# Performance work log

Hardware: AMD Instinct MI355X
Metric: run time of the kernel (lower is better)

Reference implementation:

```python
import jax, jax.numpy as jnp
import numpy as np

B, N, IN_DIM, HID, EMB, E = 64, 2048, 128, 256, 64, 4194304
TOTAL = B * N


def _init(key, shape, fan_in):
    return jax.random.normal(key, shape, jnp.float32) / np.sqrt(fan_in).astype(np.float32)


def setup_inputs() -> dict:
    key = jax.random.key(0)
    ks = jax.random.split(key, 9)
    x = jax.random.normal(ks[0], (TOTAL, IN_DIM), jnp.float32)
    src = jax.random.randint(ks[1], (E,), 0, TOTAL)
    dst = jax.random.randint(ks[2], (E,), 0, TOTAL)
    return {
        "x": x,
        "src": src,
        "dst": dst,
        "num_nodes": TOTAL,
        "nodes_per_graph": N,
        "w_lin": _init(ks[3], (IN_DIM, HID), IN_DIM),
        "b_lin": jnp.zeros((HID,), jnp.float32),
        "w_c0": _init(ks[4], (HID, HID), HID),
        "b_c0": jnp.zeros((HID,), jnp.float32),
        "w_c1": _init(ks[5], (HID, HID), HID),
        "b_c1": jnp.zeros((HID,), jnp.float32),
        "w_emb": _init(ks[6], (HID, EMB), HID),
        "b_emb": jnp.zeros((EMB,), jnp.float32),
    }


def reference(x, src, dst, num_nodes, nodes_per_graph,
              w_lin, b_lin, w_c0, b_c0, w_c1, b_c1, w_emb, b_emb):
    # DGL GraphConv norm='both': deg clamped to min 1, symmetric normalization
    ones = jnp.ones(src.shape, x.dtype)
    out_deg = jax.ops.segment_sum(ones, src, num_segments=num_nodes)
    in_deg = jax.ops.segment_sum(ones, dst, num_segments=num_nodes)
    out_norm = jnp.maximum(out_deg, 1.0) ** -0.5  # [num_nodes]
    in_norm = jnp.maximum(in_deg, 1.0) ** -0.5

    def graph_conv(h, W, b):
        hs = h * out_norm[:, None]                                   # pre-norm by out-degree
        agg = jax.ops.segment_sum(hs[src], dst, num_segments=num_nodes)  # SpMM: sum messages
        return (agg * in_norm[:, None]) @ W + b                      # post-norm, then weight

    h = jax.nn.relu(x @ w_lin + b_lin)          # [total, HID]
    h = jax.nn.relu(graph_conv(h, w_c0, b_c0))  # residual=False for agg_style='node'
    h = jax.nn.relu(graph_conv(h, w_c1, b_c1))
    # agent node 0 of each graph in the batch: indices 0, N, 2N, ...
    agent = h[jnp.arange(0, num_nodes, nodes_per_graph)]  # [B, HID]
    return agent @ w_emb + b_emb                          # [B, EMB]
```

## Files before the change

kernel.cpp:

```cpp
#include <hip/hip_runtime.h>
#include <hip/hip_bf16.h>

#define TOTAL_N   131072
#define NEDGE     4194304
#define NPG       2048
#define IN_DIM_K  128
#define HID_K     256
#define EMB_K     64
#define NAGENT    64

#define F1CAP     4096
#define APACK     128
#define BCAP      96
#define NL        8

#define G1        256
#define EPB1      (NEDGE / G1)
#define HWORDS    (TOTAL_N / 8)

#define SELB      256
#define EPB       (NEDGE / SELB)


#define ZERO_SPAN 34048

typedef float f32x4 __attribute__((ext_vector_type(4)));
typedef short bf16x8 __attribute__((ext_vector_type(8)));

__device__ inline unsigned short f2bf(float f) {
    unsigned int u = __float_as_uint(f);
    return (unsigned short)((u + 0x7FFFu + ((u >> 16) & 1u)) >> 16);
}

__global__ __launch_bounds__(1024) void k_outdeg_e0(
    const int* __restrict__ src, const int* __restrict__ dst,
    unsigned int* __restrict__ partial,
    unsigned int* __restrict__ bitmap,
    int* __restrict__ e0pack, int* __restrict__ e0cnt)
{
    __shared__ unsigned int hist[HWORDS];
    int t = threadIdx.x;
    #pragma unroll
    for (int i = 0; i < HWORDS / 1024; i++) hist[t + i * 1024] = 0u;
    __syncthreads();

    int ebase = blockIdx.x * EPB1;
    const int4* s4 = (const int4*)(src + ebase);
    const int4* d4 = (const int4*)(dst + ebase);
    #pragma unroll
    for (int i = 0; i < EPB1 / 4096; i++) {
        int4 sv = s4[i * 1024 + t];
        int4 dv = d4[i * 1024 + t];
        int ss[4] = {sv.x, sv.y, sv.z, sv.w};
        int dd[4] = {dv.x, dv.y, dv.z, dv.w};
        #pragma unroll
        for (int j = 0; j < 4; j++) {
            int s = ss[j], d = dd[j];
            atomicAdd(&hist[s >> 3], 1u << ((s & 7) * 4));
            if ((d & (NPG - 1)) == 0) {
                atomicOr(&bitmap[s >> 5], 1u << (s & 31));
                int a = d >> 11;
                int slot = atomicAdd(&e0cnt[a], 1);
                if (slot < APACK) e0pack[a * APACK + slot] = s;
            }
        }
    }
    __syncthreads();
    unsigned int* pout = partial + blockIdx.x * HWORDS;
    #pragma unroll
    for (int i = 0; i < HWORDS / 1024; i++) pout[t + i * 1024] = hist[t + i * 1024];
}

__global__ __launch_bounds__(1024) void k_auxred(
    const unsigned int* __restrict__ bitmap, int* __restrict__ loc,
    int* __restrict__ counters,
    const unsigned int* __restrict__ partial, unsigned int* __restrict__ out_deg,
    const float* __restrict__ wlin, unsigned short* __restrict__ wswz)
{
    int b = blockIdx.x;
    int t = threadIdx.x;
    if (b < 128) {
        __shared__ int cnt, gbase;
        if (t == 0) cnt = 0;
        __syncthreads();
        int v = b * 1024 + t;
        int f = (bitmap[v >> 5] >> (v & 31)) & 1u;
        int p = -1;
        if (f) p = atomicAdd(&cnt, 1);
        __syncthreads();
        if (t == 0) gbase = cnt ? atomicAdd(&counters[1], cnt) : 0;
        __syncthreads();
        int l = -1;
        if (p >= 0) { int id = gbase + p; if (id < F1CAP) l = id; }
        loc[v] = l;
    } else if (b < 256) {
        __shared__ unsigned int redE[8][128], redO[8][128];
        int wl = t & 127, gs = t >> 7;
        int w = (b - 128) * 128 + wl;
        unsigned int accE = 0, accO = 0;
        #pragma unroll 8
        for (int i = 0; i < 32; i++) {
            unsigned int v = partial[(gs * 32 + i) * HWORDS + w];
            accE += v & 0x0F0F0F0Fu;
            accO += (v >> 4) & 0x0F0F0F0Fu;
        }
        redE[gs][wl] = accE;
        redO[gs][wl] = accO;
        __syncthreads();
        if (gs == 0) {
            unsigned int sE = 0, sO = 0;
            #pragma unroll
            for (int j = 0; j < 8; j++) { sE += redE[j][wl]; sO += redO[j][wl]; }
            uint4 lo = make_uint4(sE & 255u, sO & 255u, (sE >> 8) & 255u, (sO >> 8) & 255u);
            uint4 hi = make_uint4((sE >> 16) & 255u, (sO >> 16) & 255u, (sE >> 24) & 255u, (sO >> 24) & 255u);
            ((uint4*)(out_deg + 8 * w))[0] = lo;
            ((uint4*)(out_deg + 8 * w))[1] = hi;
        }
    } else {
        int g = (b - 256) * 1024 + t;
        int lane = g & 63, ct = (g >> 6) & 15, kt = g >> 10;
        int colbase = ct * 16 + (lane & 15);
        int kbase = kt * 32 + (lane >> 4) * 8;
        unsigned short o[8];
        #pragma unroll
        for (int i = 0; i < 8; i++) o[i] = f2bf(wlin[(kbase + i) * HID_K + colbase]);
        *(ushort4*)(wswz + g * 8)     = make_ushort4(o[0], o[1], o[2], o[3]);
        *(ushort4*)(wswz + g * 8 + 4) = make_ushort4(o[4], o[5], o[6], o[7]);
    }
}

__global__ __launch_bounds__(1024) void k_e1_select(
    const int* __restrict__ src, const int* __restrict__ dst,
    const int* __restrict__ loc, const unsigned int* __restrict__ bitmap,
    int* __restrict__ inF1, int* __restrict__ es_bucket)
{
    __shared__ unsigned int bm[TOTAL_N / 32];
    int t = threadIdx.x;
    ((uint4*)bm)[t] = ((const uint4*)bitmap)[t];
    __syncthreads();

    int ebase = blockIdx.x * EPB;
    const int4* d4p = (const int4*)(dst + ebase);
    #pragma unroll
    for (int i = 0; i < EPB / 4096; i++) {
        int4 d4 = d4p[i * 1024 + t];
        int eidx = ebase + (i * 1024 + t) * 4;
        int dd[4] = {d4.x, d4.y, d4.z, d4.w};
        #pragma unroll
        for (int j = 0; j < 4; j++) {
            int d = dd[j];
            if ((bm[d >> 5] >> (d & 31)) & 1u) {
                int l = loc[d];
                if (l >= 0) {
                    int slot = atomicAdd(&inF1[l], 1);
                    if (slot < BCAP) es_bucket[l * BCAP + slot] = src[eidx + j];
                }
            }
        }
    }
}

__global__ __launch_bounds__(256) void k_h0h1(
    const float* __restrict__ x, const unsigned short* __restrict__ wswz,
    const float* __restrict__ blin, const int* __restrict__ es_bucket,
    const unsigned int* __restrict__ out_deg, const int* __restrict__ inF1,
    const int* __restrict__ counters,
    const float* __restrict__ wc0, const float* __restrict__ bc0,
    float* __restrict__ h1)
{
    __shared__ unsigned short A[32][136];
    __shared__ float as[NL][HID_K];
    __shared__ float escs[32];
    __shared__ int rsrc[32];

    int nF1 = min(counters[1], F1CAP);
    int base = blockIdx.x * NL;
    if (base >= nF1) return;
    int t = threadIdx.x;
    int lane = t & 63, wq = t >> 6;
    int cbase = lane & 15, rgrp = (lane >> 4) * 4;

    bf16x8 bfrag[4][4];
    #pragma unroll
    for (int kt = 0; kt < 4; kt++)
        #pragma unroll
        for (int n = 0; n < 4; n++)
            bfrag[kt][n] = *(const bf16x8*)(wswz + ((kt * 16 + wq * 4 + n) * 64 + lane) * 8);

    float bj[4];
    #pragma unroll
    for (int n = 0; n < 4; n++) bj[n] = blin[wq * 64 + n * 16 + cbase];

    for (int r = 0; r < NL; r++) {
        int l = base + r;
        int cnt = (l < nF1) ? min(inF1[l], BCAP) : 0;
        float colacc[4] = {0.f, 0.f, 0.f, 0.f};
        int ntile = (cnt + 31) >> 5;

        for (int ti = 0; ti < ntile; ti++) {
            __syncthreads();
            if (t < 32) {
                int rr = ti * 32 + t;
                int s = (rr < cnt) ? es_bucket[l * BCAP + rr] : -1;
                rsrc[t] = s;
                escs[t] = (s >= 0) ? rsqrtf((float)max((int)out_deg[s], 1)) : 0.f;
            }
            __syncthreads();
            #pragma unroll
            for (int i = 0; i < 4; i++) {
                int idx = t + i * 256;
                int rr = idx >> 5, q = idx & 31;
                int s = rsrc[rr];
                float4 v = make_float4(0.f, 0.f, 0.f, 0.f);
                if (s >= 0) v = ((const float4*)(x + (long long)s * IN_DIM_K))[q];
                ushort4 h;
                h.x = f2bf(v.x); h.y = f2bf(v.y); h.z = f2bf(v.z); h.w = f2bf(v.w);
                *(ushort4*)&A[rr][q * 4] = h;
            }
            __syncthreads();

            f32x4 acc[2][4];
            #pragma unroll
            for (int m = 0; m < 2; m++)
                #pragma unroll
                for (int n = 0; n < 4; n++) acc[m][n] = (f32x4){0.f, 0.f, 0.f, 0.f};

            const unsigned short* Ab = &A[0][0];
            #pragma unroll
            for (int kt = 0; kt < 4; kt++) {
                bf16x8 a0 = *(const bf16x8*)(Ab + ((lane & 15) * 136 + kt * 32 + (lane >> 4) * 8));
                bf16x8 a1 = *(const bf16x8*)(Ab + (((lane & 15) + 16) * 136 + kt * 32 + (lane >> 4) * 8));
                #pragma unroll
                for (int n = 0; n < 4; n++) {
                    acc[0][n] = __builtin_amdgcn_mfma_f32_16x16x32_bf16(a0, bfrag[kt][n], acc[0][n], 0, 0, 0);
                    acc[1][n] = __builtin_amdgcn_mfma_f32_16x16x32_bf16(a1, bfrag[kt][n], acc[1][n], 0, 0, 0);
                }
            }

            #pragma unroll
            for (int n = 0; n < 4; n++) {
                float part = 0.f;
                #pragma unroll
                for (int m = 0; m < 2; m++)
                    #pragma unroll
                    for (int j = 0; j < 4; j++) {
                        int row = m * 16 + rgrp + j;
                        part += fmaxf(acc[m][n][j] + bj[n], 0.f) * escs[row];
                    }
                part += __shfl_xor(part, 16);
                part += __shfl_xor(part, 32);
                colacc[n] += part;
            }
        }

        float ns = (l < nF1) ? rsqrtf((float)max(inF1[l], 1)) : 0.f;
        if (lane < 16) {
            #pragma unroll
            for (int n = 0; n < 4; n++)
                as[r][wq * 64 + n * 16 + lane] = colacc[n] * ns;
        }
    }
    __syncthreads();

    float acc8[NL];
    #pragma unroll
    for (int e = 0; e < NL; e++) acc8[e] = 0.f;
    int j = t;
    for (int k = 0; k < HID_K; k += 4) {
        float w0 = wc0[(k + 0) * HID_K + j];
        float w1 = wc0[(k + 1) * HID_K + j];
        float w2 = wc0[(k + 2) * HID_K + j];
        float w3 = wc0[(k + 3) * HID_K + j];
        #pragma unroll
        for (int e = 0; e < NL; e++) {
            float4 av = *(const float4*)&as[e][k];
            acc8[e] = fmaf(av.x, w0, acc8[e]);
            acc8[e] = fmaf(av.y, w1, acc8[e]);
            acc8[e] = fmaf(av.z, w2, acc8[e]);
            acc8[e] = fmaf(av.w, w3, acc8[e]);
        }
    }
    float bcj = bc0[j];
    #pragma unroll
    for (int e = 0; e < NL; e++) {
        int l = base + e;
        if (l < nF1) h1[(long long)l * HID_K + j] = fmaxf(acc8[e] + bcj, 0.f);
    }
}

__global__ __launch_bounds__(256) void k_final(
    const int* __restrict__ e0pack, const int* __restrict__ e0cnt,
    const int* __restrict__ loc, const unsigned int* __restrict__ out_deg,
    const float* __restrict__ h1,
    const float* __restrict__ wc1, const float* __restrict__ bc1,
    const float* __restrict__ wemb, const float* __restrict__ bemb,
    float* __restrict__ out)
{
    __shared__ float a_s[HID_K];
    __shared__ float h2[HID_K];
    __shared__ int   ls[APACK];
    __shared__ float scs[APACK];
    int a = blockIdx.x;
    int t = threadIdx.x;

    int n0 = e0cnt[a];
    int ne = min(n0, APACK);
    if (t < ne) {
        int s = e0pack[a * APACK + t];
        int l = loc[s];
        ls[t] = l;
        scs[t] = (l >= 0) ? rsqrtf((float)max((int)out_deg[s], 1)) : 0.f;
    }
    __syncthreads();

    float acc = 0.f;
    for (int i = 0; i < ne; i++) {
        int l = ls[i];
        if (l >= 0) acc = fmaf(scs[i], h1[(long long)l * HID_K + t], acc);
    }
    a_s[t] = acc * rsqrtf((float)max(n0, 1));
    __syncthreads();

    float h = 0.f;
    for (int k = 0; k < HID_K; k++)
        h = fmaf(a_s[k], wc1[k * HID_K + t], h);
    h2[t] = fmaxf(h + bc1[t], 0.f);
    __syncthreads();

    if (t < EMB_K) {
        float o = bemb[t];
        for (int k = 0; k < HID_K; k++)
            o = fmaf(h2[k], wemb[k * EMB_K + t], o);
        out[a * EMB_K + t] = o;
    }
}

extern "C" void kernel_launch(void* const* d_in, const int* in_sizes, int n_in,
                              void* d_out, int out_size, void* d_ws, size_t ws_size,
                              hipStream_t stream)
{
    const float* x    = (const float*)d_in[0];
    const int*   src  = (const int*)d_in[1];
    const int*   dst  = (const int*)d_in[2];
    const float* wlin = (const float*)d_in[5];
    const float* blin = (const float*)d_in[6];
    const float* wc0  = (const float*)d_in[7];
    const float* bc0  = (const float*)d_in[8];
    const float* wc1  = (const float*)d_in[9];
    const float* bc1  = (const float*)d_in[10];
    const float* wemb = (const float*)d_in[11];
    const float* bemb = (const float*)d_in[12];
    float* out = (float*)d_out;

    char* ws = (char*)d_ws;
    int*            counters  = (int*)(ws + 0);
    int*            inF1      = (int*)(ws + 1024);
    int*            e0cnt     = (int*)(ws + 17408);
    unsigned int*   bitmap    = (unsigned int*)(ws + 17664);
    int*            loc       = (int*)(ws + 65536);
    int*            e0pack    = (int*)(ws + 589824);
    int*            es_bucket = (int*)(ws + 622592);
    unsigned int*   out_deg   = (unsigned int*)(ws + 2195456);
    unsigned short* wswz      = (unsigned short*)(ws + 2719744);
    float*          h1        = (float*)(ws + 2785280);
    unsigned int*   partial   = (unsigned int*)(ws + 6979584);

    hipMemsetAsync(ws, 0, ZERO_SPAN, stream);

    k_outdeg_e0<<<G1, 1024, 0, stream>>>(src, dst, partial, bitmap, e0pack, e0cnt);
    k_auxred<<<260, 1024, 0, stream>>>(bitmap, loc, counters,
                                       partial, out_deg, wlin, wswz);
    k_e1_select<<<SELB, 1024, 0, stream>>>(src, dst, loc, bitmap,
                                           inF1, es_bucket);
    k_h0h1<<<F1CAP / NL, 256, 0, stream>>>(x, wswz, blin, es_bucket, out_deg,
                                           inF1, counters, wc0, bc0, h1);
    k_final<<<NAGENT, 256, 0, stream>>>(e0pack, e0cnt, loc, out_deg, h1,
                                        wc1, bc1, wemb, bemb, out);
}
```

Measured before the change: 118.3 us.

## Process four F1 nodes in parallel per 1024-thread block in k_h0h1

Restructures k_h0h1 so each 1024-thread block holds four 256-thread groups. Each group handles one frontier node at the same time, where before a single 256-thread block looped over eight nodes in sequence. The bf16 weight fragments are now loaded from global memory inside the MFMA loop rather than kept in registers, which lowers register pressure for the larger block. The goal is to shorten the serial per-block chain and raise parallelism. The costs are more reloads of wswz and padding work, because every group runs tmax tiles and block-wide syncs make all four groups wait on the slowest node.

```diff
diff --git a/kernel.cpp b/kernel.cpp
--- a/kernel.cpp
+++ b/kernel.cpp
@@ -12,7 +12,7 @@
 #define F1CAP     4096
 #define APACK     128
 #define BCAP      96
-#define NL        8
+#define NGRP      4
 
 #define G1        256
 #define EPB1      (NEDGE / G1)
@@ -160,7 +160,7 @@
     }
 }
 
-__global__ __launch_bounds__(256) void k_h0h1(
+__global__ __launch_bounds__(1024) void k_h0h1(
     const float* __restrict__ x, const unsigned short* __restrict__ wswz,
     const float* __restrict__ blin, const int* __restrict__ es_bucket,
     const unsigned int* __restrict__ out_deg, const int* __restrict__ inF1,
@@ -168,124 +168,107 @@
     const float* __restrict__ wc0, const float* __restrict__ bc0,
     float* __restrict__ h1)
 {
-    __shared__ unsigned short A[32][136];
-    __shared__ float as[NL][HID_K];
-    __shared__ float escs[32];
-    __shared__ int rsrc[32];
+    __shared__ unsigned short A[NGRP][32][136];
+    __shared__ float as[NGRP][260];
+    __shared__ float escs[NGRP][32];
+    __shared__ int rsrc[NGRP][32];
+    __shared__ int ntl[NGRP];
 
     int nF1 = min(counters[1], F1CAP);
-    int base = blockIdx.x * NL;
+    int base = blockIdx.x * NGRP;
     if (base >= nF1) return;
     int t = threadIdx.x;
-    int lane = t & 63, wq = t >> 6;
+    int g = t >> 8, tt = t & 255;
+    int lane = tt & 63, wq = tt >> 6;
     int cbase = lane & 15, rgrp = (lane >> 4) * 4;
-
-    bf16x8 bfrag[4][4];
-    #pragma unroll
-    for (int kt = 0; kt < 4; kt++)
-        #pragma unroll
-        for (int n = 0; n < 4; n++)
-            bfrag[kt][n] = *(const bf16x8*)(wswz + ((kt * 16 + wq * 4 + n) * 64 + lane) * 8);
+    int l = base + g;
+    int cnt = (l < nF1) ? min(inF1[l], BCAP) : 0;
+
+    if (tt == 0) ntl[g] = (cnt + 31) >> 5;
+    __syncthreads();
+    int tmax = max(max(ntl[0], ntl[1]), max(ntl[2], ntl[3]));
 
     float bj[4];
     #pragma unroll
     for (int n = 0; n < 4; n++) bj[n] = blin[wq * 64 + n * 16 + cbase];
 
-    for (int r = 0; r < NL; r++) {
-        int l = base + r;
-        int cnt = (l < nF1) ? min(inF1[l], BCAP) : 0;
-        float colacc[4] = {0.f, 0.f, 0.f, 0.f};
-        int ntile = (cnt + 31) >> 5;
-
-        for (int ti = 0; ti < ntile; ti++) {
-            __syncthreads();
-            if (t < 32) {
-                int rr = ti * 32 + t;
-                int s = (rr < cnt) ? es_bucket[l * BCAP + rr] : -1;
-                rsrc[t] = s;
-                escs[t] = (s >= 0) ? rsqrtf((float)max((int)out_deg[s], 1)) : 0.f;
+    float colacc[4] = {0.f, 0.f, 0.f, 0.f};
+
+    for (int ti = 0; ti < tmax; ti++) {
+        __syncthreads();
+        if (tt < 32) {
+            int rr = ti * 32 + tt;
+            int s = (rr < cnt) ? es_bucket[l * BCAP + rr] : -1;
+            rsrc[g][tt] = s;
+            escs[g][tt] = (s >= 0) ? rsqrtf((float)max((int)out_deg[s], 1)) : 0.f;
+        }
+        __syncthreads();
+        #pragma unroll
+        for (int i = 0; i < 4; i++) {
+            int idx = tt + i * 256;
+            int rr = idx >> 5, q = idx & 31;
+            int s = rsrc[g][rr];
+            float4 v = make_float4(0.f, 0.f, 0.f, 0.f);
+            if (s >= 0) v = ((const float4*)(x + (long long)s * IN_DIM_K))[q];
+            ushort4 h;
+            h.x = f2bf(v.x); h.y = f2bf(v.y); h.z = f2bf(v.z); h.w = f2bf(v.w);
+            *(ushort4*)&A[g][rr][q * 4] = h;
+        }
+        __syncthreads();
+
+        f32x4 acc[2][4];
+        #pragma unroll
+        for (int m = 0; m < 2; m++)
+            #pragma unroll
+            for (int n = 0; n < 4; n++) acc[m][n] = (f32x4){0.f, 0.f, 0.f, 0.f};
+
+        const unsigned short* Ab = &A[g][0][0];
+        #pragma unroll
+        for (int kt = 0; kt < 4; kt++) {
+            bf16x8 a0 = *(const bf16x8*)(Ab + ((lane & 15) * 136 + kt * 32 + (lane >> 4) * 8));
+            bf16x8 a1 = *(const bf16x8*)(Ab + (((lane & 15) + 16) * 136 + kt * 32 + (lane >> 4) * 8));
+            #pragma unroll
+            for (int n = 0; n < 4; n++) {
+                bf16x8 bf = *(const bf16x8*)(wswz + ((kt * 16 + wq * 4 + n) * 64 + lane) * 8);
+                acc[0][n] = __builtin_amdgcn_mfma_f32_16x16x32_bf16(a0, bf, acc[0][n], 0, 0, 0);
+                acc[1][n] = __builtin_amdgcn_mfma_f32_16x16x32_bf16(a1, bf, acc[1][n], 0, 0, 0);
             }
-            __syncthreads();
-            #pragma unroll
-            for (int i = 0; i < 4; i++) {
-                int idx = t + i * 256;
-                int rr = idx >> 5, q = idx & 31;
-                int s = rsrc[rr];
-                float4 v = make_float4(0.f, 0.f, 0.f, 0.f);
-                if (s >= 0) v = ((const float4*)(x + (long long)s * IN_DIM_K))[q];
-                ushort4 h;
-                h.x = f2bf(v.x); h.y = f2bf(v.y); h.z = f2bf(v.z); h.w = f2bf(v.w);
-                *(ushort4*)&A[rr][q * 4] = h;
-            }
-            __syncthreads();
-
-            f32x4 acc[2][4];
+        }
+
+        #pragma unroll
+        for (int n = 0; n < 4; n++) {
+            float part = 0.f;
             #pragma unroll
             for (int m = 0; m < 2; m++)
                 #pragma unroll
-                for (int n = 0; n < 4; n++) acc[m][n] = (f32x4){0.f, 0.f, 0.f, 0.f};
-
-            const unsigned short* Ab = &A[0][0];
-            #pragma unroll
-            for (int kt = 0; kt < 4; kt++) {
-                bf16x8 a0 = *(const bf16x8*)(Ab + ((lane & 15) * 136 + kt * 32 + (lane >> 4) * 8));
-                bf16x8 a1 = *(const bf16x8*)(Ab + (((lane & 15) + 16) * 136 + kt * 32 + (lane >> 4) * 8));
-                #pragma unroll
-                for (int n = 0; n < 4; n++) {
-                    acc[0][n] = __builtin_amdgcn_mfma_f32_16x16x32_bf16(a0, bfrag[kt][n], acc[0][n], 0, 0, 0);
-                    acc[1][n] = __builtin_amdgcn_mfma_f32_16x16x32_bf16(a1, bfrag[kt][n], acc[1][n], 0, 0, 0);
+                for (int j = 0; j < 4; j++) {
+                    int row = m * 16 + rgrp + j;
+                    part += fmaxf(acc[m][n][j] + bj[n], 0.f) * escs[g][row];
                 }
-            }
-
-            #pragma unroll
-            for (int n = 0; n < 4; n++) {
-                float part = 0.f;
-                #pragma unroll
-                for (int m = 0; m < 2; m++)
-                    #pragma unroll
-                    for (int j = 0; j < 4; j++) {
-                        int row = m * 16 + rgrp + j;
-                        part += fmaxf(acc[m][n][j] + bj[n], 0.f) * escs[row];
-                    }
-                part += __shfl_xor(part, 16);
-                part += __shfl_xor(part, 32);
-                colacc[n] += part;
-            }
-        }
-
-        float ns = (l < nF1) ? rsqrtf((float)max(inF1[l], 1)) : 0.f;
-        if (lane < 16) {
-            #pragma unroll
-            for (int n = 0; n < 4; n++)
-                as[r][wq * 64 + n * 16 + lane] = colacc[n] * ns;
-        }
-    }
-    __syncthreads();
-
-    float acc8[NL];
-    #pragma unroll
-    for (int e = 0; e < NL; e++) acc8[e] = 0.f;
-    int j = t;
+            part += __shfl_xor(part, 16);
+            part += __shfl_xor(part, 32);
+            colacc[n] += part;
+        }
+    }
+
+    float ns = (l < nF1) ? rsqrtf((float)max(inF1[l], 1)) : 0.f;
+    if (lane < 16) {
+        #pragma unroll
+        for (int n = 0; n < 4; n++)
+            as[g][wq * 64 + n * 16 + lane] = colacc[n] * ns;
+    }
+    __syncthreads();
+
+    float acc1 = 0.f;
+    int j = tt;
     for (int k = 0; k < HID_K; k += 4) {
-        float w0 = wc0[(k + 0) * HID_K + j];
-        float w1 = wc0[(k + 1) * HID_K + j];
-        float w2 = wc0[(k + 2) * HID_K + j];
-        float w3 = wc0[(k + 3) * HID_K + j];
-        #pragma unroll
-        for (int e = 0; e < NL; e++) {
-            float4 av = *(const float4*)&as[e][k];
-            acc8[e] = fmaf(av.x, w0, acc8[e]);
-            acc8[e] = fmaf(av.y, w1, acc8[e]);
-            acc8[e] = fmaf(av.z, w2, acc8[e]);
-            acc8[e] = fmaf(av.w, w3, acc8[e]);
-        }
-    }
-    float bcj = bc0[j];
-    #pragma unroll
-    for (int e = 0; e < NL; e++) {
-        int l = base + e;
-        if (l < nF1) h1[(long long)l * HID_K + j] = fmaxf(acc8[e] + bcj, 0.f);
-    }
+        float4 av = *(const float4*)&as[g][k];
+        acc1 = fmaf(av.x, wc0[(k + 0) * HID_K + j], acc1);
+        acc1 = fmaf(av.y, wc0[(k + 1) * HID_K + j], acc1);
+        acc1 = fmaf(av.z, wc0[(k + 2) * HID_K + j], acc1);
+        acc1 = fmaf(av.w, wc0[(k + 3) * HID_K + j], acc1);
+    }
+    if (l < nF1) h1[(long long)l * HID_K + j] = fmaxf(acc1 + bc0[j], 0.f);
 }
 
 __global__ __launch_bounds__(256) void k_final(
@@ -372,8 +355,8 @@
                                        partial, out_deg, wlin, wswz);
     k_e1_select<<<SELB, 1024, 0, stream>>>(src, dst, loc, bitmap,
                                            inF1, es_bucket);
-    k_h0h1<<<F1CAP / NL, 256, 0, stream>>>(x, wswz, blin, es_bucket, out_deg,
-                                           inF1, counters, wc0, bc0, h1);
+    k_h0h1<<<F1CAP / NGRP, 1024, 0, stream>>>(x, wswz, blin, es_bucket, out_deg,
+                                              inF1, counters, wc0, bc0, h1);
     k_final<<<NAGENT, 256, 0, stream>>>(e0pack, e0cnt, loc, out_deg, h1,
                                         wc1, bc1, wemb, bemb, out);
 }
```

After: 136.7 us. 1.16x slower.
